# Kernel tuning notes

Measured on AMD Instinct MI355X. Metric: run time of the kernel, lower is better.

## Reference

```python
import jax, jax.numpy as jnp
import numpy as np

NUM_REL = 3


def _edge_norm(dst, et, n_nodes):
    # PyG RGCNConv default aggr='mean': mean over edges per (dst, relation).
    seg = dst * NUM_REL + et
    cnt = jax.ops.segment_sum(jnp.ones(dst.shape[0], jnp.float32), seg,
                              num_segments=n_nodes * NUM_REL)
    return 1.0 / jnp.maximum(cnt, 1.0)[seg], seg  # [E]


def _rgcn_layer(x, W, root, b, src, dst, et, norm_e, seg, transform_first):
    n = x.shape[0]
    if transform_first:
        # h_r = x @ W_r for all relations, gather message per edge, scatter-add.
        H = jnp.einsum('ni,rio->rno', x, W)          # [R, N, out]
        m = H[et, src] * norm_e[:, None]             # [E, out]
        agg = jax.ops.segment_sum(m, dst, num_segments=n)
    else:
        # mean-aggregate in input space first (mean commutes with linear map).
        m = x[src] * norm_e[:, None]                 # [E, in]
        A = jax.ops.segment_sum(m, seg, num_segments=n * NUM_REL)
        A = A.reshape(n, NUM_REL, -1)                # [N, R, in]
        agg = jnp.einsum('nri,rio->no', A, W)
    return agg + x @ root + b


def _make_params(key, in_c, out_c):
    dims = [(in_c, 1024), (1024, 512), (512, 128)]
    ks = jax.random.split(key, 14)
    p = {}
    for li, (i, o) in enumerate(dims, start=1):
        p[f'W{li}'] = jax.random.normal(ks[3 * li - 3], (NUM_REL, i, o), jnp.float32) * 0.02
        p[f'root{li}'] = jax.random.normal(ks[3 * li - 2], (i, o), jnp.float32) * 0.02
        p[f'b{li}'] = jnp.zeros((o,), jnp.float32)
    p['fc_w'] = jax.random.normal(ks[9], (128, out_c), jnp.float32) * 0.02
    p['fc_b'] = jnp.zeros((out_c,), jnp.float32)
    return p


def setup_inputs() -> dict:
    key = jax.random.key(0)
    N, E, IN_C, OUT_C = 40000, 500000, 256, 21
    k1, k2, k3, k4 = jax.random.split(key, 4)
    inp = {
        'x': jax.random.normal(k1, (N, IN_C), jnp.float32),
        'edge_index': jax.random.randint(k2, (2, E), 0, N, jnp.int64)
            if jax.config.jax_enable_x64 else jax.random.randint(k2, (2, E), 0, N, jnp.int32),
        'edge_type': jax.random.randint(k3, (E,), 0, NUM_REL, jnp.int32),
    }
    inp.update(_make_params(k4, IN_C, OUT_C))
    return inp


def reference(x, edge_index, edge_type, W1, root1, b1, W2, root2, b2,
              W3, root3, b3, fc_w, fc_b):
    src, dst = edge_index[0], edge_index[1]
    et = edge_type
    n = x.shape[0]
    norm_e, seg = _edge_norm(dst, et, n)
    # layer 1: in(256) < out(1024) -> aggregate-first is cheaper
    h = _rgcn_layer(x, W1, root1, b1, src, dst, et, norm_e, seg, transform_first=False)
    h = jax.nn.relu(h)  # dropout is identity in eval mode
    # layer 2: in(1024) > out(512) -> transform-first
    h = _rgcn_layer(h, W2, root2, b2, src, dst, et, norm_e, seg, transform_first=True)
    h = jax.nn.relu(h)
    # layer 3: in(512) > out(128) -> transform-first
    h = _rgcn_layer(h, W3, root3, b3, src, dst, et, norm_e, seg, transform_first=True)
    h = jax.nn.relu(h)
    logits = h @ fc_w + fc_b
    return jax.nn.log_softmax(logits, axis=1)
```

## Files before the change

### kernel.cpp

```cpp
#include <hip/hip_runtime.h>
#include <cstdint>
#include <cstddef>


typedef short bf16x8 __attribute__((ext_vector_type(8)));
typedef float f32x4 __attribute__((ext_vector_type(4)));

#define GF_BIAS 1
#define GF_RELU 2
#define GF_BF16 4

__device__ __forceinline__ unsigned short f2bf(float f) {
    unsigned u = __float_as_uint(f);
    return (unsigned short)((u + 0x7FFFu + ((u >> 16) & 1u)) >> 16);
}
__device__ __forceinline__ float bf2f(unsigned short h) {
    return __uint_as_float((unsigned)h << 16);
}

__global__ __launch_bounds__(256) void zero_kernel(float* __restrict__ p, long n4)
{
    long i = (long)blockIdx.x * 256 + threadIdx.x;
    if (i < n4) ((float4*)p)[i] = make_float4(0.f, 0.f, 0.f, 0.f);
}

__global__ __launch_bounds__(256) void count_kernel(
    const int* __restrict__ dst, const int* __restrict__ et,
    int* __restrict__ cnt, int E)
{
    int e = blockIdx.x * 256 + threadIdx.x;
    if (e < E) atomicAdd(&cnt[dst[e] * 3 + et[e]], 1);
}

__global__ __launch_bounds__(256) void scanA(
    const int* __restrict__ cnt, int* __restrict__ base,
    int* __restrict__ bsum, int S)
{
    __shared__ int sh[256];
    int i = blockIdx.x * 256 + threadIdx.x;
    int v = (i < S) ? cnt[i] : 0;
    sh[threadIdx.x] = v;
    __syncthreads();
#pragma unroll
    for (int off = 1; off < 256; off <<= 1) {
        int t = (threadIdx.x >= off) ? sh[threadIdx.x - off] : 0;
        __syncthreads();
        sh[threadIdx.x] += t;
        __syncthreads();
    }
    if (i < S) base[i] = sh[threadIdx.x] - v;
    if (threadIdx.x == 255) bsum[blockIdx.x] = sh[255];
}

__global__ __launch_bounds__(512) void scanB(int* __restrict__ bsum, int NB)
{
    __shared__ int sh[512];
    int t = threadIdx.x;
    int v = (t < NB) ? bsum[t] : 0;
    sh[t] = v;
    __syncthreads();
#pragma unroll
    for (int off = 1; off < 512; off <<= 1) {
        int u = (t >= off) ? sh[t - off] : 0;
        __syncthreads();
        sh[t] += u;
        __syncthreads();
    }
    if (t < NB) bsum[t] = sh[t] - v;
}

__global__ __launch_bounds__(256) void scanC(
    int* __restrict__ base, const int* __restrict__ bsum, int S)
{
    int i = blockIdx.x * 256 + threadIdx.x;
    if (i < S) base[i] += bsum[blockIdx.x];
}

__global__ __launch_bounds__(256) void fill_kernel(
    const int* __restrict__ src, const int* __restrict__ dst,
    const int* __restrict__ et, const int* __restrict__ base,
    int* __restrict__ ecur, int* __restrict__ elist, int E)
{
    int e = blockIdx.x * 256 + threadIdx.x;
    if (e >= E) return;
    int seg = dst[e] * 3 + et[e];
    int pos = base[seg] + atomicAdd(&ecur[seg], 1);
    elist[pos] = src[e];
}

__global__ __launch_bounds__(256) void transpose_bf16(
    const float* __restrict__ in, unsigned short* __restrict__ out,
    int R, int C, int ldo)
{
    int idx = blockIdx.x * 256 + threadIdx.x;
    if (idx >= R * C) return;
    int j = idx / R, i = idx - j * R;
    out[(size_t)j * ldo + i] = f2bf(in[(size_t)i * C + j]);
}

__global__ __launch_bounds__(256) void conv_bf16(
    const float* __restrict__ s, unsigned short* __restrict__ d, long n8)
{
    long i = (long)blockIdx.x * 256 + threadIdx.x;
    if (i >= n8) return;
    const float* p = s + i * 8;
    float4 a = *(const float4*)p, b = *(const float4*)(p + 4);
    ushort4 o0, o1;
    o0.x = f2bf(a.x); o0.y = f2bf(a.y); o0.z = f2bf(a.z); o0.w = f2bf(a.w);
    o1.x = f2bf(b.x); o1.y = f2bf(b.y); o1.z = f2bf(b.z); o1.w = f2bf(b.w);
    *(ushort4*)(d + i * 8) = o0;
    *(ushort4*)(d + i * 8 + 4) = o1;
}

__global__ __launch_bounds__(256) void make_bias(
    float* __restrict__ dst, const float* __restrict__ src, int nsrc, int ntot)
{
    int i = blockIdx.x * 256 + threadIdx.x;
    if (i < ntot) dst[i] = (i < nsrc) ? src[i] : 0.f;
}

__global__ __launch_bounds__(256) void agg1_kernel(
    const unsigned short* __restrict__ xb, const int* __restrict__ base,
    const int* __restrict__ cnt, const int* __restrict__ elist,
    unsigned short* __restrict__ Xcat)
{
    int n = blockIdx.x;
    int w = threadIdx.x >> 6, l = threadIdx.x & 63;
    if (w == 3) {
        *(ushort4*)&Xcat[(size_t)n * 1024 + 768 + l * 4] =
            *(const ushort4*)&xb[(size_t)n * 256 + l * 4];
        return;
    }
    int seg = n * 3 + w;
    int st = base[seg], len = cnt[seg];
    float norm = 1.0f / (float)(len > 0 ? len : 1);
    float4 s = make_float4(0.f, 0.f, 0.f, 0.f);
    for (int i = 0; i < len; ++i) {
        int sx = elist[st + i];
        ushort4 v = *(const ushort4*)&xb[(size_t)sx * 256 + l * 4];
        s.x += bf2f(v.x); s.y += bf2f(v.y); s.z += bf2f(v.z); s.w += bf2f(v.w);
    }
    ushort4 o;
    o.x = f2bf(s.x * norm); o.y = f2bf(s.y * norm);
    o.z = f2bf(s.z * norm); o.w = f2bf(s.w * norm);
    *(ushort4*)&Xcat[(size_t)n * 1024 + w * 256 + l * 4] = o;
}

__global__ __launch_bounds__(128) void agg2_fused(
    const unsigned short* __restrict__ H2all, unsigned short* __restrict__ h2b,
    const int* __restrict__ base, const int* __restrict__ cnt,
    const int* __restrict__ elist)
{
    int n = blockIdx.x, t = threadIdx.x;
    ushort4 rv = *(const ushort4*)&H2all[(size_t)n * 2048 + t * 4];
    float4 a = make_float4(bf2f(rv.x), bf2f(rv.y), bf2f(rv.z), bf2f(rv.w));
#pragma unroll
    for (int r = 0; r < 3; ++r) {
        int seg = n * 3 + r;
        int st = base[seg], len = cnt[seg];
        float norm = 1.0f / (float)(len > 0 ? len : 1);
        float4 s = make_float4(0.f, 0.f, 0.f, 0.f);
        for (int i = 0; i < len; ++i) {
            int sx = elist[st + i];
            ushort4 v = *(const ushort4*)&H2all[(size_t)sx * 2048 + 512 * (1 + r) + t * 4];
            s.x += bf2f(v.x); s.y += bf2f(v.y); s.z += bf2f(v.z); s.w += bf2f(v.w);
        }
        a.x += s.x * norm; a.y += s.y * norm; a.z += s.z * norm; a.w += s.w * norm;
    }
    ushort4 o;
    o.x = f2bf(fmaxf(a.x, 0.f)); o.y = f2bf(fmaxf(a.y, 0.f));
    o.z = f2bf(fmaxf(a.z, 0.f)); o.w = f2bf(fmaxf(a.w, 0.f));
    *(ushort4*)&h2b[(size_t)n * 512 + t * 4] = o;
}

__global__ __launch_bounds__(128) void agg2_inc(
    const unsigned short* __restrict__ H2q, float* __restrict__ h2acc,
    unsigned short* __restrict__ h2b, const int* __restrict__ base,
    const int* __restrict__ cnt, const int* __restrict__ elist, int r, int last)
{
    int n = blockIdx.x, t = threadIdx.x;
    int seg = n * 3 + r;
    int st = base[seg], len = cnt[seg];
    float norm = 1.0f / (float)(len > 0 ? len : 1);
    float4 s = make_float4(0.f, 0.f, 0.f, 0.f);
    for (int i = 0; i < len; ++i) {
        int sx = elist[st + i];
        ushort4 v = *(const ushort4*)&H2q[(size_t)sx * 512 + t * 4];
        s.x += bf2f(v.x); s.y += bf2f(v.y); s.z += bf2f(v.z); s.w += bf2f(v.w);
    }
    float4 a = *(const float4*)&h2acc[(size_t)n * 512 + t * 4];
    a.x += s.x * norm; a.y += s.y * norm; a.z += s.z * norm; a.w += s.w * norm;
    if (!last) {
        *(float4*)&h2acc[(size_t)n * 512 + t * 4] = a;
    } else {
        ushort4 o;
        o.x = f2bf(fmaxf(a.x, 0.f)); o.y = f2bf(fmaxf(a.y, 0.f));
        o.z = f2bf(fmaxf(a.z, 0.f)); o.w = f2bf(fmaxf(a.w, 0.f));
        *(ushort4*)&h2b[(size_t)n * 512 + t * 4] = o;
    }
}

__global__ __launch_bounds__(64) void agg3_kernel(
    const unsigned short* __restrict__ H3cat, float* __restrict__ h3,
    const int* __restrict__ base, const int* __restrict__ cnt,
    const int* __restrict__ elist)
{
    int n = blockIdx.x;
    int l = threadIdx.x;
    ushort2 rt = *(const ushort2*)&H3cat[(size_t)n * 512 + l * 2];
    float s0 = bf2f(rt.x), s1 = bf2f(rt.y);
#pragma unroll
    for (int r = 0; r < 3; ++r) {
        int seg = n * 3 + r;
        int st = base[seg], len = cnt[seg];
        float norm = 1.0f / (float)(len > 0 ? len : 1);
        float t0 = 0.f, t1 = 0.f;
        for (int i = 0; i < len; ++i) {
            int sx = elist[st + i];
            ushort2 v = *(const ushort2*)&H3cat[(size_t)sx * 512 + 128 * (1 + r) + l * 2];
            t0 += bf2f(v.x); t1 += bf2f(v.y);
        }
        s0 += t0 * norm; s1 += t1 * norm;
    }
    float2 o; o.x = s0; o.y = s1;
    *(float2*)&h3[(size_t)n * 128 + l * 2] = o;
}

__global__ __launch_bounds__(256) void gemm_mfma(
    const unsigned short* __restrict__ A, const unsigned short* __restrict__ Bt,
    const float* __restrict__ bias, void* __restrict__ C,
    int Nout, int K, int ldbt, int flags, int lgGX)
{
    __shared__ short __align__(16) As[8192];
    __shared__ short __align__(16) Bs[8192];
    const int tid = threadIdx.x;
    const int w = tid >> 6, l = tid & 63;

    const int nblk = (int)gridDim.x;
    const int q = nblk >> 3, rem = nblk & 7;
    const int xcd = blockIdx.x & 7, local = blockIdx.x >> 3;
    const int id2 = xcd * q + (xcd < rem ? xcd : rem) + local;
    const int row0 = (id2 >> lgGX) * 128;
    const int col0 = (id2 & ((1 << lgGX) - 1)) * 128;

    const int wm = w >> 1, wn = w & 1;
    const int lr = l >> 3, lc = l & 7;

    f32x4 acc[4][4];
#pragma unroll
    for (int i = 0; i < 4; ++i)
#pragma unroll
        for (int j = 0; j < 4; ++j) acc[i][j] = (f32x4){0.f, 0.f, 0.f, 0.f};

    for (int k0 = 0; k0 < K; k0 += 64) {
        __syncthreads();
#pragma unroll
        for (int i = 0; i < 4; ++i) {
            const int c  = i * 4 + w;
            const int r  = c * 8 + lr;
            const int c8 = lc ^ (r & 7);
            __builtin_amdgcn_global_load_lds(
                (const __attribute__((address_space(1))) void*)
                    (A + (size_t)(row0 + r) * K + k0 + c8 * 8),
                (__attribute__((address_space(3))) void*)(As + c * 512),
                16, 0, 0);
            __builtin_amdgcn_global_load_lds(
                (const __attribute__((address_space(1))) void*)
                    (Bt + (size_t)(col0 + r) * ldbt + k0 + c8 * 8),
                (__attribute__((address_space(3))) void*)(Bs + c * 512),
                16, 0, 0);
        }
        __syncthreads();
#pragma unroll
        for (int ks = 0; ks < 2; ++ks) {
            bf16x8 af[4], bfv[4];
#pragma unroll
            for (int mf = 0; mf < 4; ++mf) {
                int r = wm * 64 + mf * 16 + (l & 15);
                int byt = (r * 128 + ks * 64 + (l >> 4) * 16) ^ ((r & 7) << 4);
                af[mf] = *(const bf16x8*)((const char*)As + byt);
            }
#pragma unroll
            for (int nf = 0; nf < 4; ++nf) {
                int r = wn * 64 + nf * 16 + (l & 15);
                int byt = (r * 128 + ks * 64 + (l >> 4) * 16) ^ ((r & 7) << 4);
                bfv[nf] = *(const bf16x8*)((const char*)Bs + byt);
            }
#pragma unroll
            for (int mf = 0; mf < 4; ++mf)
#pragma unroll
                for (int nf = 0; nf < 4; ++nf)
                    acc[mf][nf] = __builtin_amdgcn_mfma_f32_16x16x32_bf16(
                        af[mf], bfv[nf], acc[mf][nf], 0, 0, 0);
        }
    }

    const int lrow = (l >> 4) * 4;
    const int lcol = l & 15;
#pragma unroll
    for (int mf = 0; mf < 4; ++mf) {
#pragma unroll
        for (int nf = 0; nf < 4; ++nf) {
            int col = col0 + wn * 64 + nf * 16 + lcol;
            float bv = (flags & GF_BIAS) ? bias[col] : 0.f;
#pragma unroll
            for (int rr = 0; rr < 4; ++rr) {
                int row = row0 + wm * 64 + mf * 16 + lrow + rr;
                float v = acc[mf][nf][rr] + bv;
                if (flags & GF_RELU) v = fmaxf(v, 0.f);
                size_t idx = (size_t)row * Nout + col;
                if (flags & GF_BF16) ((unsigned short*)C)[idx] = f2bf(v);
                else                 ((float*)C)[idx] = v;
            }
        }
    }
}

__global__ __launch_bounds__(256) void head_kernel(
    const float* __restrict__ h3, const float* __restrict__ fcw,
    const float* __restrict__ fcb, float* __restrict__ out, int M)
{
    __shared__ float sh[4][128];
    int wid = threadIdx.x >> 6, lane = threadIdx.x & 63;
    int row = blockIdx.x * 4 + wid;
    sh[wid][lane]      = fmaxf(h3[(size_t)row * 128 + lane], 0.f);
    sh[wid][64 + lane] = fmaxf(h3[(size_t)row * 128 + 64 + lane], 0.f);
    __syncthreads();
    float logit = 0.f;
    if (lane < 21) {
        logit = fcb[lane];
#pragma unroll
        for (int k = 0; k < 128; ++k) logit += sh[wid][k] * fcw[k * 21 + lane];
    }
    float v = (lane < 21) ? logit : -INFINITY;
#pragma unroll
    for (int off = 32; off; off >>= 1) v = fmaxf(v, __shfl_xor(v, off));
    float mx = v;
    float ex = (lane < 21) ? expf(logit - mx) : 0.f;
#pragma unroll
    for (int off = 32; off; off >>= 1) ex += __shfl_xor(ex, off);
    if (lane < 21) out[(size_t)row * 21 + lane] = logit - mx - logf(ex);
}

extern "C" void kernel_launch(void* const* d_in, const int* in_sizes, int n_in,
                              void* d_out, int out_size, void* d_ws, size_t ws_size,
                              hipStream_t stream)
{
    const float* x     = (const float*)d_in[0];
    const int*   ei    = (const int*)d_in[1];
    const int*   etp   = (const int*)d_in[2];
    const float* W1    = (const float*)d_in[3];
    const float* root1 = (const float*)d_in[4];
    const float* b1    = (const float*)d_in[5];
    const float* W2    = (const float*)d_in[6];
    const float* root2 = (const float*)d_in[7];
    const float* b2    = (const float*)d_in[8];
    const float* W3    = (const float*)d_in[9];
    const float* root3 = (const float*)d_in[10];
    const float* b3    = (const float*)d_in[11];
    const float* fcw   = (const float*)d_in[12];
    const float* fcb   = (const float*)d_in[13];
    float* out = (float*)d_out;
    (void)n_in; (void)out_size;

    const int N  = in_sizes[0] / 256;
    const int E  = in_sizes[2];
    const int S  = N * 3;
    const int NP = (N + 127) / 128 * 128;
    const int GY = NP / 128;
    const int NB = (S + 255) / 256;
    const int* srcp = ei;
    const int* dstp = ei + E;

    const size_t SZ_X1024 = (size_t)NP * 1024 * 2;
    const size_t SZ_X512b = (size_t)NP * 512 * 2;
    const size_t SZ_X2048 = (size_t)NP * 2048 * 2;
    const size_t SZ_XB    = (size_t)NP * 256 * 2;
    const size_t SZ_H3    = (size_t)NP * 128 * 4;

    char* ws = (char*)d_ws;
    int*            cnt   = (int*)(ws + 0);
    int*            base  = (int*)(ws + 480256);
    int*            elist = (int*)(ws + 960512);
    float*          b2cat = (float*)(ws + 2960512);
    float*          b3cat = (float*)(ws + 2968704);
    unsigned short* W3cat = (unsigned short*)(ws + 2970752);
    unsigned short* W2cat = (unsigned short*)(ws + 3495040);
    const size_t fixed_end = 7689344;
    const size_t FUSED_NEED = 7692288 + SZ_X2048 + SZ_X1024;
    const bool fused = ws_size >= FUSED_NEED;

    char* arena;
    unsigned short *W1t, *xb, *Xcat, *h1b, *H2all, *H2q, *h2b, *H3cat;
    float *h2acc, *h3;
    if (fused) {
        arena = ws + 7692288;
        Xcat  = (unsigned short*)(arena);
        W1t   = (unsigned short*)(arena + SZ_X1024);
        xb    = (unsigned short*)(arena + SZ_X1024 + 2097152);
        h1b   = (unsigned short*)(arena + SZ_X2048);
        H2all = (unsigned short*)(arena);
        h2b   = (unsigned short*)(arena + SZ_X2048);
        H3cat = (unsigned short*)(arena);
        h3    = (float*)(arena + SZ_X512b);
        H2q = nullptr; h2acc = nullptr;
    } else {
        W1t   = (unsigned short*)(ws + fixed_end);
        arena = ws + fixed_end + 2097152 + 2944;
        Xcat  = (unsigned short*)(arena);
        h2acc = (float*)(arena);
        h1b   = (unsigned short*)(arena + SZ_X1024);
        h2b   = (unsigned short*)(arena + SZ_X1024);
        H3cat = (unsigned short*)(arena + SZ_X1024 + SZ_X512b);
        xb    = (unsigned short*)(arena + 2 * SZ_X1024);
        H2q   = (unsigned short*)(arena + 2 * SZ_X1024);
        h3    = (float*)(arena + 2 * SZ_X1024);
        H2all = nullptr;
    }
    int* ecur = (int*)(arena);
    int* bsum = (int*)(arena + 480256);

    zero_kernel<<<(S * 4 / 16 + 255) / 256, 256, 0, stream>>>((float*)cnt, S * 4 / 16);
    zero_kernel<<<(S * 4 / 16 + 255) / 256, 256, 0, stream>>>((float*)ecur, S * 4 / 16);
    count_kernel<<<(E + 255) / 256, 256, 0, stream>>>(dstp, etp, cnt, E);
    scanA<<<NB, 256, 0, stream>>>(cnt, base, bsum, S);
    scanB<<<1, 512, 0, stream>>>(bsum, NB);
    scanC<<<NB, 256, 0, stream>>>(base, bsum, S);
    fill_kernel<<<(E + 255) / 256, 256, 0, stream>>>(srcp, dstp, etp, base, ecur, elist, E);

    transpose_bf16<<<(768 * 1024 + 255) / 256, 256, 0, stream>>>(W1, W1t, 768, 1024, 1024);
    transpose_bf16<<<(256 * 1024 + 255) / 256, 256, 0, stream>>>(root1, W1t + 768, 256, 1024, 1024);
    transpose_bf16<<<(1024 * 512 + 255) / 256, 256, 0, stream>>>(root2, W2cat, 1024, 512, 1024);
    for (int r = 0; r < 3; ++r)
        transpose_bf16<<<(1024 * 512 + 255) / 256, 256, 0, stream>>>(
            W2 + (size_t)r * 524288, W2cat + (size_t)(1 + r) * 524288, 1024, 512, 1024);
    transpose_bf16<<<(512 * 128 + 255) / 256, 256, 0, stream>>>(root3, W3cat, 512, 128, 512);
    for (int r = 0; r < 3; ++r)
        transpose_bf16<<<(512 * 128 + 255) / 256, 256, 0, stream>>>(
            W3 + (size_t)r * 65536, W3cat + (size_t)(1 + r) * 65536, 512, 128, 512);
    make_bias<<<8, 256, 0, stream>>>(b2cat, b2, 512, 2048);
    make_bias<<<2, 256, 0, stream>>>(b3cat, b3, 128, 512);
    conv_bf16<<<(int)(((long)N * 32 + 255) / 256), 256, 0, stream>>>(x, xb, (long)N * 32);

    agg1_kernel<<<N, 256, 0, stream>>>(xb, base, cnt, elist, Xcat);
    gemm_mfma<<<8 * GY, 256, 0, stream>>>(
        Xcat, W1t, b1, h1b, 1024, 1024, 1024, GF_BIAS | GF_RELU | GF_BF16, 3);

    if (fused) {
        gemm_mfma<<<16 * GY, 256, 0, stream>>>(
            h1b, W2cat, b2cat, H2all, 2048, 1024, 1024, GF_BIAS | GF_BF16, 4);
        agg2_fused<<<N, 128, 0, stream>>>(H2all, h2b, base, cnt, elist);
    } else {
        gemm_mfma<<<4 * GY, 256, 0, stream>>>(
            h1b, W2cat, b2, h2acc, 512, 1024, 1024, GF_BIAS, 2);
        for (int r = 0; r < 3; ++r) {
            gemm_mfma<<<4 * GY, 256, 0, stream>>>(
                h1b, W2cat + (size_t)(1 + r) * 524288, nullptr, H2q, 512, 1024, 1024, GF_BF16, 2);
            agg2_inc<<<N, 128, 0, stream>>>(H2q, h2acc, h2b, base, cnt, elist, r, r == 2);
        }
    }

    gemm_mfma<<<4 * GY, 256, 0, stream>>>(
        h2b, W3cat, b3cat, H3cat, 512, 512, 512, GF_BIAS | GF_BF16, 2);
    agg3_kernel<<<N, 64, 0, stream>>>(H3cat, h3, base, cnt, elist);

    head_kernel<<<N / 4, 256, 0, stream>>>(h3, fcw, fcb, out, N);
}
```

Measured before the change: 705.4 us.

## Use 256x256 double-buffered GEMM, fuse layer-3 aggregation with head, merge prep kernels

The 128x128 single-buffered MFMA GEMM is replaced by a 512-thread 256x256-tile kernel. It double-buffers LDS through global_load_lds with explicit vmcnt waits and raises wave priority around the MFMA blocks. The CSR fill now decrements the count array in place and adds a sentinel, so segment lengths come from base differences and the second zero/cursor buffer is no longer needed. The weight transposes and bias concatenations are merged into fewer launches, and agg3 is fused with the log-softmax head so h3 never goes through global memory. The larger tiles raise per-block LDS and register pressure and may leave fewer blocks on the grid for the smaller GEMMs.

```diff
diff --git a/kernel.cpp b/kernel.cpp
--- a/kernel.cpp
+++ b/kernel.cpp
@@ -78,24 +78,57 @@
 
 __global__ __launch_bounds__(256) void fill_kernel(
     const int* __restrict__ src, const int* __restrict__ dst,
-    const int* __restrict__ et, const int* __restrict__ base,
-    int* __restrict__ ecur, int* __restrict__ elist, int E)
+    const int* __restrict__ et, int* __restrict__ base,
+    int* __restrict__ cnt, int* __restrict__ elist, int E, int S)
 {
     int e = blockIdx.x * 256 + threadIdx.x;
+    if (e == 0) base[S] = E;
     if (e >= E) return;
     int seg = dst[e] * 3 + et[e];
-    int pos = base[seg] + atomicAdd(&ecur[seg], 1);
-    elist[pos] = src[e];
-}
-
-__global__ __launch_bounds__(256) void transpose_bf16(
-    const float* __restrict__ in, unsigned short* __restrict__ out,
-    int R, int C, int ldo)
+    int old = atomicSub(&cnt[seg], 1);
+    elist[base[seg] + old - 1] = src[e];
+}
+
+__global__ __launch_bounds__(256) void tr_w1(
+    const float* __restrict__ W1, const float* __restrict__ root1,
+    unsigned short* __restrict__ W1t)
 {
     int idx = blockIdx.x * 256 + threadIdx.x;
-    if (idx >= R * C) return;
-    int j = idx / R, i = idx - j * R;
-    out[(size_t)j * ldo + i] = f2bf(in[(size_t)i * C + j]);
+    int j = idx >> 10, k = idx & 1023;
+    float v = (k < 768) ? W1[(size_t)k * 1024 + j]
+                        : root1[(size_t)(k - 768) * 1024 + j];
+    W1t[(size_t)j * 1024 + k] = f2bf(v);
+}
+
+__global__ __launch_bounds__(256) void tr_w2f(
+    const float* __restrict__ root2, const float* __restrict__ W2,
+    unsigned short* __restrict__ W2cat)
+{
+    int idx = blockIdx.x * 256 + threadIdx.x;
+    int row = idx >> 10, k = idx & 1023;
+    int s = row >> 9, j = row & 511;
+    const float* src = (s == 0) ? root2 : W2 + (size_t)(s - 1) * 524288;
+    W2cat[(size_t)row * 1024 + k] = f2bf(src[(size_t)k * 512 + j]);
+}
+
+__global__ __launch_bounds__(256) void tr_w3f(
+    const float* __restrict__ root3, const float* __restrict__ W3,
+    unsigned short* __restrict__ W3cat)
+{
+    int idx = blockIdx.x * 256 + threadIdx.x;
+    int row = idx >> 9, k = idx & 511;
+    int s = row >> 7, j = row & 127;
+    const float* src = (s == 0) ? root3 : W3 + (size_t)(s - 1) * 65536;
+    W3cat[(size_t)row * 512 + k] = f2bf(src[(size_t)k * 128 + j]);
+}
+
+__global__ __launch_bounds__(256) void bias_cat(
+    float* __restrict__ b2cat, float* __restrict__ b3cat,
+    const float* __restrict__ b2, const float* __restrict__ b3)
+{
+    int i = blockIdx.x * 256 + threadIdx.x;
+    if (i < 2048) b2cat[i] = (i < 512) ? b2[i] : 0.f;
+    else if (i < 2560) { int j = i - 2048; b3cat[j] = (j < 128) ? b3[j] : 0.f; }
 }
 
 __global__ __launch_bounds__(256) void conv_bf16(
@@ -112,17 +145,9 @@
     *(ushort4*)(d + i * 8 + 4) = o1;
 }
 
-__global__ __launch_bounds__(256) void make_bias(
-    float* __restrict__ dst, const float* __restrict__ src, int nsrc, int ntot)
-{
-    int i = blockIdx.x * 256 + threadIdx.x;
-    if (i < ntot) dst[i] = (i < nsrc) ? src[i] : 0.f;
-}
-
 __global__ __launch_bounds__(256) void agg1_kernel(
     const unsigned short* __restrict__ xb, const int* __restrict__ base,
-    const int* __restrict__ cnt, const int* __restrict__ elist,
-    unsigned short* __restrict__ Xcat)
+    const int* __restrict__ elist, unsigned short* __restrict__ Xcat)
 {
     int n = blockIdx.x;
     int w = threadIdx.x >> 6, l = threadIdx.x & 63;
@@ -132,7 +157,7 @@
         return;
     }
     int seg = n * 3 + w;
-    int st = base[seg], len = cnt[seg];
+    int st = base[seg], len = base[seg + 1] - st;
     float norm = 1.0f / (float)(len > 0 ? len : 1);
     float4 s = make_float4(0.f, 0.f, 0.f, 0.f);
     for (int i = 0; i < len; ++i) {
@@ -148,8 +173,7 @@
 
 __global__ __launch_bounds__(128) void agg2_fused(
     const unsigned short* __restrict__ H2all, unsigned short* __restrict__ h2b,
-    const int* __restrict__ base, const int* __restrict__ cnt,
-    const int* __restrict__ elist)
+    const int* __restrict__ base, const int* __restrict__ elist)
 {
     int n = blockIdx.x, t = threadIdx.x;
     ushort4 rv = *(const ushort4*)&H2all[(size_t)n * 2048 + t * 4];
@@ -157,7 +181,7 @@
 #pragma unroll
     for (int r = 0; r < 3; ++r) {
         int seg = n * 3 + r;
-        int st = base[seg], len = cnt[seg];
+        int st = base[seg], len = base[seg + 1] - st;
         float norm = 1.0f / (float)(len > 0 ? len : 1);
         float4 s = make_float4(0.f, 0.f, 0.f, 0.f);
         for (int i = 0; i < len; ++i) {
@@ -176,11 +200,11 @@
 __global__ __launch_bounds__(128) void agg2_inc(
     const unsigned short* __restrict__ H2q, float* __restrict__ h2acc,
     unsigned short* __restrict__ h2b, const int* __restrict__ base,
-    const int* __restrict__ cnt, const int* __restrict__ elist, int r, int last)
+    const int* __restrict__ elist, int r, int last)
 {
     int n = blockIdx.x, t = threadIdx.x;
     int seg = n * 3 + r;
-    int st = base[seg], len = cnt[seg];
+    int st = base[seg], len = base[seg + 1] - st;
     float norm = 1.0f / (float)(len > 0 ? len : 1);
     float4 s = make_float4(0.f, 0.f, 0.f, 0.f);
     for (int i = 0; i < len; ++i) {
@@ -200,146 +224,174 @@
     }
 }
 
-__global__ __launch_bounds__(64) void agg3_kernel(
-    const unsigned short* __restrict__ H3cat, float* __restrict__ h3,
-    const int* __restrict__ base, const int* __restrict__ cnt,
-    const int* __restrict__ elist)
-{
-    int n = blockIdx.x;
-    int l = threadIdx.x;
-    ushort2 rt = *(const ushort2*)&H3cat[(size_t)n * 512 + l * 2];
+__global__ __launch_bounds__(256) void agg3_head(
+    const unsigned short* __restrict__ H3cat, const float* __restrict__ fcw,
+    const float* __restrict__ fcb, const int* __restrict__ base,
+    const int* __restrict__ elist, float* __restrict__ out)
+{
+    __shared__ float sh[4][128];
+    int wid = threadIdx.x >> 6, lane = threadIdx.x & 63;
+    int n = blockIdx.x * 4 + wid;
+    ushort2 rt = *(const ushort2*)&H3cat[(size_t)n * 512 + lane * 2];
     float s0 = bf2f(rt.x), s1 = bf2f(rt.y);
 #pragma unroll
     for (int r = 0; r < 3; ++r) {
         int seg = n * 3 + r;
-        int st = base[seg], len = cnt[seg];
+        int st = base[seg], len = base[seg + 1] - st;
         float norm = 1.0f / (float)(len > 0 ? len : 1);
         float t0 = 0.f, t1 = 0.f;
         for (int i = 0; i < len; ++i) {
             int sx = elist[st + i];
-            ushort2 v = *(const ushort2*)&H3cat[(size_t)sx * 512 + 128 * (1 + r) + l * 2];
+            ushort2 v = *(const ushort2*)&H3cat[(size_t)sx * 512 + 128 * (1 + r) + lane * 2];
             t0 += bf2f(v.x); t1 += bf2f(v.y);
         }
         s0 += t0 * norm; s1 += t1 * norm;
     }
-    float2 o; o.x = s0; o.y = s1;
-    *(float2*)&h3[(size_t)n * 128 + l * 2] = o;
-}
-
-__global__ __launch_bounds__(256) void gemm_mfma(
+    sh[wid][lane * 2]     = fmaxf(s0, 0.f);
+    sh[wid][lane * 2 + 1] = fmaxf(s1, 0.f);
+    __syncthreads();
+    float logit = 0.f;
+    if (lane < 21) {
+        logit = fcb[lane];
+#pragma unroll
+        for (int k = 0; k < 128; ++k) logit += sh[wid][k] * fcw[k * 21 + lane];
+    }
+    float v = (lane < 21) ? logit : -INFINITY;
+#pragma unroll
+    for (int off = 32; off; off >>= 1) v = fmaxf(v, __shfl_xor(v, off));
+    float mx = v;
+    float ex = (lane < 21) ? expf(logit - mx) : 0.f;
+#pragma unroll
+    for (int off = 32; off; off >>= 1) ex += __shfl_xor(ex, off);
+    if (lane < 21) out[(size_t)n * 21 + lane] = logit - mx - logf(ex);
+}
+
+__global__ __launch_bounds__(512) void gemm256(
     const unsigned short* __restrict__ A, const unsigned short* __restrict__ Bt,
     const float* __restrict__ bias, void* __restrict__ C,
-    int Nout, int K, int ldbt, int flags, int lgGX)
-{
-    __shared__ short __align__(16) As[8192];
-    __shared__ short __align__(16) Bs[8192];
+    int M, int Nout, int K, int flags, int lgGX)
+{
+    __shared__ char smem[131072];
     const int tid = threadIdx.x;
     const int w = tid >> 6, l = tid & 63;
+    const int wm = w >> 2, wn = w & 3;
 
     const int nblk = (int)gridDim.x;
     const int q = nblk >> 3, rem = nblk & 7;
     const int xcd = blockIdx.x & 7, local = blockIdx.x >> 3;
     const int id2 = xcd * q + (xcd < rem ? xcd : rem) + local;
-    const int row0 = (id2 >> lgGX) * 128;
-    const int col0 = (id2 & ((1 << lgGX) - 1)) * 128;
-
-    const int wm = w >> 1, wn = w & 1;
-    const int lr = l >> 3, lc = l & 7;
-
-    f32x4 acc[4][4];
-#pragma unroll
-    for (int i = 0; i < 4; ++i)
-#pragma unroll
-        for (int j = 0; j < 4; ++j) acc[i][j] = (f32x4){0.f, 0.f, 0.f, 0.f};
-
-    for (int k0 = 0; k0 < K; k0 += 64) {
-        __syncthreads();
-#pragma unroll
-        for (int i = 0; i < 4; ++i) {
-            const int c  = i * 4 + w;
-            const int r  = c * 8 + lr;
-            const int c8 = lc ^ (r & 7);
+    const int row0 = (id2 >> lgGX) * 256;
+    const int col0 = (id2 & ((1 << lgGX) - 1)) * 256;
+    const int NT = K >> 6;
+
+    auto stage_half = [&](const unsigned short* P, int ld, int rbase, int rclamp,
+                          int k0, int ldsoff) {
+#pragma unroll
+        for (int i = 0; i < 2; ++i) {
+            int r = w * 8 + i * 64 + (l >> 3);
+            int gr = rbase + r; gr = gr > rclamp ? rclamp : gr;
+            int so = (l & 7) ^ (r & 7);
             __builtin_amdgcn_global_load_lds(
                 (const __attribute__((address_space(1))) void*)
-                    (A + (size_t)(row0 + r) * K + k0 + c8 * 8),
-                (__attribute__((address_space(3))) void*)(As + c * 512),
+                    (P + (size_t)gr * ld + k0 + so * 8),
+                (__attribute__((address_space(3))) void*)
+                    (smem + ldsoff + (w * 64 + i * 512) * 16),
                 16, 0, 0);
-            __builtin_amdgcn_global_load_lds(
-                (const __attribute__((address_space(1))) void*)
-                    (Bt + (size_t)(col0 + r) * ldbt + k0 + c8 * 8),
-                (__attribute__((address_space(3))) void*)(Bs + c * 512),
-                16, 0, 0);
-        }
-        __syncthreads();
-#pragma unroll
-        for (int ks = 0; ks < 2; ++ks) {
-            bf16x8 af[4], bfv[4];
-#pragma unroll
-            for (int mf = 0; mf < 4; ++mf) {
-                int r = wm * 64 + mf * 16 + (l & 15);
-                int byt = (r * 128 + ks * 64 + (l >> 4) * 16) ^ ((r & 7) << 4);
-                af[mf] = *(const bf16x8*)((const char*)As + byt);
+        }
+    };
+    auto stage_tile = [&](int kt) {
+        int bb = (kt & 1) << 16;
+        int k0 = kt << 6;
+        stage_half(A, K, row0,        M - 1,    k0, bb);
+        stage_half(A, K, row0 + 128,  M - 1,    k0, bb + 16384);
+        stage_half(Bt, K, col0,       Nout - 1, k0, bb + 32768);
+        stage_half(Bt, K, col0 + 128, Nout - 1, k0, bb + 49152);
+    };
+
+    f32x4 acc[8][4];
+#pragma unroll
+    for (int i = 0; i < 8; ++i)
+#pragma unroll
+        for (int j = 0; j < 4; ++j) acc[i][j] = (f32x4){0.f, 0.f, 0.f, 0.f};
+
+    stage_tile(0);
+    stage_tile(1);
+    asm volatile("s_waitcnt vmcnt(8)" ::: "memory");
+    __builtin_amdgcn_s_barrier();
+    asm volatile("" ::: "memory");
+
+    for (int kt = 0; kt < NT; ++kt) {
+        const int bb = (kt & 1) << 16;
+        const char* Ah = smem + bb + wm * 16384;
+        const char* Bh = smem + bb + 32768 + (wn >> 1) * 16384;
+        const int rlB = (wn & 1) * 64;
+
+        bf16x8 bfr[4][2];
+#pragma unroll
+        for (int n = 0; n < 4; ++n)
+#pragma unroll
+            for (int ks = 0; ks < 2; ++ks) {
+                int rl = rlB + n * 16 + (l & 15);
+                int byt = (rl * 128 + ks * 64 + (l >> 4) * 16) ^ ((rl & 7) << 4);
+                bfr[n][ks] = *(const bf16x8*)(Bh + byt);
             }
 #pragma unroll
-            for (int nf = 0; nf < 4; ++nf) {
-                int r = wn * 64 + nf * 16 + (l & 15);
-                int byt = (r * 128 + ks * 64 + (l >> 4) * 16) ^ ((r & 7) << 4);
-                bfv[nf] = *(const bf16x8*)((const char*)Bs + byt);
-            }
-#pragma unroll
-            for (int mf = 0; mf < 4; ++mf)
-#pragma unroll
-                for (int nf = 0; nf < 4; ++nf)
-                    acc[mf][nf] = __builtin_amdgcn_mfma_f32_16x16x32_bf16(
-                        af[mf], bfv[nf], acc[mf][nf], 0, 0, 0);
-        }
+        for (int q2 = 0; q2 < 4; ++q2) {
+            bf16x8 af[2][2];
+#pragma unroll
+            for (int mm = 0; mm < 2; ++mm)
+#pragma unroll
+                for (int ks = 0; ks < 2; ++ks) {
+                    int rl = (q2 * 2 + mm) * 16 + (l & 15);
+                    int byt = (rl * 128 + ks * 64 + (l >> 4) * 16) ^ ((rl & 7) << 4);
+                    af[mm][ks] = *(const bf16x8*)(Ah + byt);
+                }
+            __builtin_amdgcn_s_setprio(1);
+#pragma unroll
+            for (int mm = 0; mm < 2; ++mm)
+#pragma unroll
+                for (int n = 0; n < 4; ++n)
+#pragma unroll
+                    for (int ks = 0; ks < 2; ++ks)
+                        acc[q2 * 2 + mm][n] = __builtin_amdgcn_mfma_f32_16x16x32_bf16(
+                            af[mm][ks], bfr[n][ks], acc[q2 * 2 + mm][n], 0, 0, 0);
+            __builtin_amdgcn_s_setprio(0);
+        }
+
+        asm volatile("" ::: "memory");
+        __builtin_amdgcn_s_barrier();
+        asm volatile("" ::: "memory");
+        if (kt + 2 < NT) {
+            stage_tile(kt + 2);
+            asm volatile("s_waitcnt vmcnt(8)" ::: "memory");
+        } else if (kt + 1 < NT) {
+            asm volatile("s_waitcnt vmcnt(0)" ::: "memory");
+        }
+        __builtin_amdgcn_s_barrier();
+        asm volatile("" ::: "memory");
     }
 
     const int lrow = (l >> 4) * 4;
     const int lcol = l & 15;
 #pragma unroll
-    for (int mf = 0; mf < 4; ++mf) {
-#pragma unroll
-        for (int nf = 0; nf < 4; ++nf) {
-            int col = col0 + wn * 64 + nf * 16 + lcol;
+    for (int m = 0; m < 8; ++m) {
+#pragma unroll
+        for (int n = 0; n < 4; ++n) {
+            int col = col0 + wn * 64 + n * 16 + lcol;
             float bv = (flags & GF_BIAS) ? bias[col] : 0.f;
 #pragma unroll
             for (int rr = 0; rr < 4; ++rr) {
-                int row = row0 + wm * 64 + mf * 16 + lrow + rr;
-                float v = acc[mf][nf][rr] + bv;
-                if (flags & GF_RELU) v = fmaxf(v, 0.f);
-                size_t idx = (size_t)row * Nout + col;
-                if (flags & GF_BF16) ((unsigned short*)C)[idx] = f2bf(v);
-                else                 ((float*)C)[idx] = v;
+                int row = row0 + wm * 128 + m * 16 + lrow + rr;
+                if (row < M) {
+                    float v = acc[m][n][rr] + bv;
+                    if (flags & GF_RELU) v = fmaxf(v, 0.f);
+                    size_t idx = (size_t)row * Nout + col;
+                    if (flags & GF_BF16) ((unsigned short*)C)[idx] = f2bf(v);
+                    else                 ((float*)C)[idx] = v;
+                }
             }
         }
     }
-}
-
-__global__ __launch_bounds__(256) void head_kernel(
-    const float* __restrict__ h3, const float* __restrict__ fcw,
-    const float* __restrict__ fcb, float* __restrict__ out, int M)
-{
-    __shared__ float sh[4][128];
-    int wid = threadIdx.x >> 6, lane = threadIdx.x & 63;
-    int row = blockIdx.x * 4 + wid;
-    sh[wid][lane]      = fmaxf(h3[(size_t)row * 128 + lane], 0.f);
-    sh[wid][64 + lane] = fmaxf(h3[(size_t)row * 128 + 64 + lane], 0.f);
-    __syncthreads();
-    float logit = 0.f;
-    if (lane < 21) {
-        logit = fcb[lane];
-#pragma unroll
-        for (int k = 0; k < 128; ++k) logit += sh[wid][k] * fcw[k * 21 + lane];
-    }
-    float v = (lane < 21) ? logit : -INFINITY;
-#pragma unroll
-    for (int off = 32; off; off >>= 1) v = fmaxf(v, __shfl_xor(v, off));
-    float mx = v;
-    float ex = (lane < 21) ? expf(logit - mx) : 0.f;
-#pragma unroll
-    for (int off = 32; off; off >>= 1) ex += __shfl_xor(ex, off);
-    if (lane < 21) out[(size_t)row * 21 + lane] = logit - mx - logf(ex);
 }
 
 extern "C" void kernel_launch(void* const* d_in, const int* in_sizes, int n_in,
@@ -363,20 +415,18 @@
     float* out = (float*)d_out;
     (void)n_in; (void)out_size;
 
-    const int N  = in_sizes[0] / 256;
-    const int E  = in_sizes[2];
-    const int S  = N * 3;
-    const int NP = (N + 127) / 128 * 128;
-    const int GY = NP / 128;
-    const int NB = (S + 255) / 256;
+    const int N   = in_sizes[0] / 256;
+    const int E   = in_sizes[2];
+    const int S   = N * 3;
+    const int NP  = (N + 127) / 128 * 128;
+    const int GYT = (NP + 255) / 256;
+    const int NB  = (S + 255) / 256;
     const int* srcp = ei;
     const int* dstp = ei + E;
 
     const size_t SZ_X1024 = (size_t)NP * 1024 * 2;
     const size_t SZ_X512b = (size_t)NP * 512 * 2;
     const size_t SZ_X2048 = (size_t)NP * 2048 * 2;
-    const size_t SZ_XB    = (size_t)NP * 256 * 2;
-    const size_t SZ_H3    = (size_t)NP * 128 * 4;
 
     char* ws = (char*)d_ws;
     int*            cnt   = (int*)(ws + 0);
@@ -392,7 +442,7 @@
 
     char* arena;
     unsigned short *W1t, *xb, *Xcat, *h1b, *H2all, *H2q, *h2b, *H3cat;
-    float *h2acc, *h3;
+    float* h2acc;
     if (fused) {
         arena = ws + 7692288;
         Xcat  = (unsigned short*)(arena);
@@ -402,11 +452,10 @@
         H2all = (unsigned short*)(arena);
         h2b   = (unsigned short*)(arena + SZ_X2048);
         H3cat = (unsigned short*)(arena);
-        h3    = (float*)(arena + SZ_X512b);
         H2q = nullptr; h2acc = nullptr;
     } else {
         W1t   = (unsigned short*)(ws + fixed_end);
-        arena = ws + fixed_end + 2097152 + 2944;
+        arena = ws + 9789440;
         Xcat  = (unsigned short*)(arena);
         h2acc = (float*)(arena);
         h1b   = (unsigned short*)(arena + SZ_X1024);
@@ -414,55 +463,42 @@
         H3cat = (unsigned short*)(arena + SZ_X1024 + SZ_X512b);
         xb    = (unsigned short*)(arena + 2 * SZ_X1024);
         H2q   = (unsigned short*)(arena + 2 * SZ_X1024);
-        h3    = (float*)(arena + 2 * SZ_X1024);
         H2all = nullptr;
     }
-    int* ecur = (int*)(arena);
-    int* bsum = (int*)(arena + 480256);
-
-    zero_kernel<<<(S * 4 / 16 + 255) / 256, 256, 0, stream>>>((float*)cnt, S * 4 / 16);
-    zero_kernel<<<(S * 4 / 16 + 255) / 256, 256, 0, stream>>>((float*)ecur, S * 4 / 16);
+    int* bsum = (int*)(arena);
+
+    zero_kernel<<<(30016 + 255) / 256, 256, 0, stream>>>((float*)cnt, 30016);
     count_kernel<<<(E + 255) / 256, 256, 0, stream>>>(dstp, etp, cnt, E);
     scanA<<<NB, 256, 0, stream>>>(cnt, base, bsum, S);
     scanB<<<1, 512, 0, stream>>>(bsum, NB);
     scanC<<<NB, 256, 0, stream>>>(base, bsum, S);
-    fill_kernel<<<(E + 255) / 256, 256, 0, stream>>>(srcp, dstp, etp, base, ecur, elist, E);
-
-    transpose_bf16<<<(768 * 1024 + 255) / 256, 256, 0, stream>>>(W1, W1t, 768, 1024, 1024);
-    transpose_bf16<<<(256 * 1024 + 255) / 256, 256, 0, stream>>>(root1, W1t + 768, 256, 1024, 1024);
-    transpose_bf16<<<(1024 * 512 + 255) / 256, 256, 0, stream>>>(root2, W2cat, 1024, 512, 1024);
-    for (int r = 0; r < 3; ++r)
-        transpose_bf16<<<(1024 * 512 + 255) / 256, 256, 0, stream>>>(
-            W2 + (size_t)r * 524288, W2cat + (size_t)(1 + r) * 524288, 1024, 512, 1024);
-    transpose_bf16<<<(512 * 128 + 255) / 256, 256, 0, stream>>>(root3, W3cat, 512, 128, 512);
-    for (int r = 0; r < 3; ++r)
-        transpose_bf16<<<(512 * 128 + 255) / 256, 256, 0, stream>>>(
-            W3 + (size_t)r * 65536, W3cat + (size_t)(1 + r) * 65536, 512, 128, 512);
-    make_bias<<<8, 256, 0, stream>>>(b2cat, b2, 512, 2048);
-    make_bias<<<2, 256, 0, stream>>>(b3cat, b3, 128, 512);
+    fill_kernel<<<(E + 255) / 256, 256, 0, stream>>>(srcp, dstp, etp, base, cnt, elist, E, S);
+
+    tr_w1 <<<4096, 256, 0, stream>>>(W1, root1, W1t);
+    tr_w2f<<<8192, 256, 0, stream>>>(root2, W2, W2cat);
+    tr_w3f<<<1024, 256, 0, stream>>>(root3, W3, W3cat);
+    bias_cat<<<10, 256, 0, stream>>>(b2cat, b3cat, b2, b3);
     conv_bf16<<<(int)(((long)N * 32 + 255) / 256), 256, 0, stream>>>(x, xb, (long)N * 32);
 
-    agg1_kernel<<<N, 256, 0, stream>>>(xb, base, cnt, elist, Xcat);
-    gemm_mfma<<<8 * GY, 256, 0, stream>>>(
-        Xcat, W1t, b1, h1b, 1024, 1024, 1024, GF_BIAS | GF_RELU | GF_BF16, 3);
+    agg1_kernel<<<N, 256, 0, stream>>>(xb, base, elist, Xcat);
+    gemm256<<<4 * GYT, 512, 0, stream>>>(
+        Xcat, W1t, b1, h1b, NP, 1024, 1024, GF_BIAS | GF_RELU | GF_BF16, 2);
 
     if (fused) {
-        gemm_mfma<<<16 * GY, 256, 0, stream>>>(
-            h1b, W2cat, b2cat, H2all, 2048, 1024, 1024, GF_BIAS | GF_BF16, 4);
-        agg2_fused<<<N, 128, 0, stream>>>(H2all, h2b, base, cnt, elist);
+        gemm256<<<8 * GYT, 512, 0, stream>>>(
+            h1b, W2cat, b2cat, H2all, NP, 2048, 1024, GF_BIAS | GF_BF16, 3);
+        agg2_fused<<<N, 128, 0, stream>>>(H2all, h2b, base, elist);
     } else {
-        gemm_mfma<<<4 * GY, 256, 0, stream>>>(
-            h1b, W2cat, b2, h2acc, 512, 1024, 1024, GF_BIAS, 2);
+        gemm256<<<2 * GYT, 512, 0, stream>>>(
+            h1b, W2cat, b2, h2acc, NP, 512, 1024, GF_BIAS, 1);
         for (int r = 0; r < 3; ++r) {
-            gemm_mfma<<<4 * GY, 256, 0, stream>>>(
-                h1b, W2cat + (size_t)(1 + r) * 524288, nullptr, H2q, 512, 1024, 1024, GF_BF16, 2);
-            agg2_inc<<<N, 128, 0, stream>>>(H2q, h2acc, h2b, base, cnt, elist, r, r == 2);
-        }
-    }
-
-    gemm_mfma<<<4 * GY, 256, 0, stream>>>(
-        h2b, W3cat, b3cat, H3cat, 512, 512, 512, GF_BIAS | GF_BF16, 2);
-    agg3_kernel<<<N, 64, 0, stream>>>(H3cat, h3, base, cnt, elist);
-
-    head_kernel<<<N / 4, 256, 0, stream>>>(h3, fcw, fcb, out, N);
-}
+            gemm256<<<2 * GYT, 512, 0, stream>>>(
+                h1b, W2cat + (size_t)(1 + r) * 524288, nullptr, H2q, NP, 512, 1024, GF_BF16, 1);
+            agg2_inc<<<N, 128, 0, stream>>>(H2q, h2acc, h2b, base, elist, r, r == 2);
+        }
+    }
+
+    gemm256<<<2 * GYT, 512, 0, stream>>>(
+        h2b, W3cat, b3cat, H3cat, NP, 512, 512, GF_BIAS | GF_BF16, 1);
+    agg3_head<<<N / 4, 256, 0, stream>>>(H3cat, fcw, fcb, base, elist, out);
+}
```

New measurement: 814.9 us. 1.16x slower.
